# Kernel optimization log

Hardware: AMD Instinct MI355X
Metric: run time of the kernel (lower is better)

The kernel has to match this reference:

```python
import jax, jax.numpy as jnp
import numpy as np

N_NODES = 50_000
N_EDGES = 1_600_000
D = 128          # input_dim == hidden_dim
L = 3            # num_layers
NUM_GRAPHS = 64
LN_EPS = 1e-5


def setup_inputs() -> dict:
    key = jax.random.key(0)
    ks = jax.random.split(key, 12)
    x = jax.random.normal(ks[0], (N_NODES, D), dtype=jnp.float32)
    edge_index = jax.random.randint(ks[1], (2, N_EDGES), 0, N_NODES, dtype=jnp.int64)
    edge_weight = jax.random.normal(ks[2], (N_EDGES,), dtype=jnp.float32)  # signed
    batch = jnp.sort(jax.random.randint(ks[3], (N_NODES,), 0, NUM_GRAPHS, dtype=jnp.int64))
    W_pos = jax.random.normal(ks[4], (L, D, D), dtype=jnp.float32) * 0.05
    b_pos = jnp.zeros((L, D), dtype=jnp.float32)
    W_neg = jax.random.normal(ks[5], (L, D, D), dtype=jnp.float32) * 0.05
    b_neg = jnp.zeros((L, D), dtype=jnp.float32)
    ln_gamma = jnp.ones((D,), dtype=jnp.float32)
    ln_beta = jnp.zeros((D,), dtype=jnp.float32)
    return dict(x=x, edge_index=edge_index, edge_weight=edge_weight, batch=batch,
                W_pos=W_pos, b_pos=b_pos, W_neg=W_neg, b_neg=b_neg,
                ln_gamma=ln_gamma, ln_beta=ln_beta)


def gcn_conv(x, src, dst, w, W, b):
    """PyG GCNConv with edge weights: lin -> sym-normalized scatter-add -> +bias.
    Self-loops (weight 1) are handled analytically instead of appending edges.
    Edges with weight 0 contribute nothing (equivalent to sign-masking the edge set)."""
    n = x.shape[0]
    xw = x @ W                                              # [N, D]
    deg = jax.ops.segment_sum(w, dst, num_segments=n) + 1.0  # +1 for self-loop; >= 1
    dinv = jax.lax.rsqrt(deg)                                # deg^{-1/2}
    norm = dinv[src] * w * dinv[dst]                         # [E]
    agg = jax.ops.segment_sum(norm[:, None] * xw[src], dst, num_segments=n)
    agg = agg + (dinv * dinv)[:, None] * xw                  # self-loop message: xw / deg
    return agg + b


def reference(x, edge_index, edge_weight, batch, W_pos, b_pos, W_neg, b_neg, ln_gamma, ln_beta):
    src, dst = edge_index[0], edge_index[1]
    # sign-split as zero-weight edges: identical math to boolean-masked edge subsets
    w_pos = jnp.maximum(edge_weight, 0.0)
    w_neg = jnp.maximum(-edge_weight, 0.0)
    for l in range(L):
        px = gcn_conv(x, src, dst, w_pos, W_pos[l], b_pos[l])
        nx = gcn_conv(x, src, dst, w_neg, W_neg[l], b_neg[l])
        x = jax.nn.relu(px) - jax.nn.relu(nx)
    # global_mean_pool
    sums = jax.ops.segment_sum(x, batch, num_segments=NUM_GRAPHS)
    counts = jax.ops.segment_sum(jnp.ones((x.shape[0],), x.dtype), batch, num_segments=NUM_GRAPHS)
    pooled = sums / jnp.maximum(counts, 1.0)[:, None]        # [G, D]
    # LayerNorm over feature dim
    mu = pooled.mean(-1, keepdims=True)
    var = ((pooled - mu) ** 2).mean(-1, keepdims=True)
    return (pooled - mu) * jax.lax.rsqrt(var + LN_EPS) * ln_gamma + ln_beta
```

## Files before the change

kernel.cpp:

```cpp
#include <hip/hip_runtime.h>
#include <hip/hip_fp16.h>

#define D 128
#define NG 64
#define WPB 4
#define TILE 2048
#define BSH 6
#define BNODES 64
#define CAP 3072
#define MASK40 ((1ULL << 40) - 1)
#define FPSCALE 1048576.0f
#define INV_FPSCALE (1.0f / 1048576.0f)
typedef unsigned int uint;
typedef unsigned long long u64;
typedef _Float16 f16x8 __attribute__((ext_vector_type(8)));
typedef float f32x4 __attribute__((ext_vector_type(4)));

__global__ void k_prep(const float* __restrict__ x, __half* __restrict__ xo,
                       const float* __restrict__ Wp, const float* __restrict__ Wn,
                       __half* __restrict__ wpt, __half* __restrict__ wnt,
                       float* sums, float* cnt, int* bktcur,
                       int total2, int nbuk) {
    int i = blockIdx.x * blockDim.x + threadIdx.x;
    if (i < total2) {
        float2 f = ((const float2*)x)[i];
        ((__half2*)xo)[i] = __floats2half2_rn(f.x, f.y);
    }
    if (i < 3 * 128 * 128) {
        int l = i >> 14;
        int r = i & 16383;
        int col = r >> 7, k = r & 127;
        size_t src = ((size_t)l << 14) + ((size_t)k << 7) + col;
        wpt[i] = __float2half_rn(Wp[src]);
        wnt[i] = __float2half_rn(Wn[src]);
    }
    if (i < NG * D) sums[i] = 0.0f;
    if (i < NG) cnt[i] = 0.0f;
    if (i < nbuk) bktcur[i] = i * CAP;
}

__global__ __launch_bounds__(256) void k_bucket(const int* __restrict__ ei,
                                                const float* __restrict__ ew,
                                                int* bktcur, uint2* rec,
                                                int E, int nbuk) {
    __shared__ int h[1024];
    __shared__ int cur[1024];
    int t = threadIdx.x;
    for (int b = t; b < 1024; b += 256) h[b] = 0;
    __syncthreads();
    int lo = blockIdx.x * TILE, hi = min(E, lo + TILE);
    for (int e = lo + t; e < hi; e += 256)
        atomicAdd(&h[ei[(size_t)E + e] >> BSH], 1);
    __syncthreads();
    for (int b = t; b < nbuk; b += 256)
        if (h[b]) cur[b] = atomicAdd(&bktcur[b], h[b]);
    __syncthreads();
    for (int e = lo + t; e < hi; e += 256) {
        int dst = ei[(size_t)E + e];
        int src = ei[e];
        float w = ew[e];
        int bkt = dst >> BSH;
        int pos = atomicAdd(&cur[bkt], 1);
        if (pos < (bkt + 1) * CAP)
            rec[pos] = make_uint2((uint)src | ((uint)(dst & (BNODES - 1)) << 16),
                                  __float_as_uint(w));
    }
}

__global__ __launch_bounds__(256) void k_deg(const uint2* __restrict__ rec,
                                             const int* __restrict__ bktcur,
                                             float2* dpn, int* row_ptr,
                                             int* cend, int* cpos, int n) {
    __shared__ u64 accp[BNODES], accn[BNODES];
    int b = blockIdx.x, t = threadIdx.x;
    if (t < BNODES) { accp[t] = 0ULL; accn[t] = 0ULL; }
    __syncthreads();
    int lo = b * CAP, hi = bktcur[b];
    for (int i = lo + t; i < hi; i += 256) {
        uint2 r = rec[i];
        int dl = (r.x >> 16) & (BNODES - 1);
        float w = __uint_as_float(r.y);
        u64 pkt = (1ULL << 40) | (u64)(fabsf(w) * FPSCALE + 0.5f);
        atomicAdd((w < 0.0f) ? &accn[dl] : &accp[dl], pkt);
    }
    __syncthreads();
    if (t < BNODES) {
        u64 p = accp[t], q = accn[t];
        int cp = (int)(p >> 40), cn = (int)(q >> 40);
        int cnt_t = cp + cn;
        int v = cnt_t;
        for (int off = 1; off < BNODES; off <<= 1) {
            int u = __shfl_up(v, off);
            if (t >= off) v += u;
        }
        int node = b * BNODES + t;
        if (node < n) {
            int base = b * CAP + v - cnt_t;
            row_ptr[node] = base;
            cend[node] = base + cnt_t;
            cpos[node] = cp;
            float2 dd;
            dd.x = rsqrtf(1.0f + (float)(p & MASK40) * INV_FPSCALE);
            dd.y = rsqrtf(1.0f + (float)(q & MASK40) * INV_FPSCALE);
            dpn[node] = dd;
        }
    }
}

__global__ __launch_bounds__(256) void k_csr(const uint2* __restrict__ rec,
                                             const int* __restrict__ bktcur,
                                             const int* __restrict__ row_ptr,
                                             const int* __restrict__ cpos,
                                             const float2* __restrict__ dpn,
                                             uint* pack, int n) {
    __shared__ int curp[BNODES], curn[BNODES];
    int b = blockIdx.x, t = threadIdx.x;
    if (t < BNODES) {
        int node = b * BNODES + t;
        if (node < n) {
            int rp = row_ptr[node];
            curp[t] = rp;
            curn[t] = rp + cpos[node];
        } else { curp[t] = 0; curn[t] = 0; }
    }
    __syncthreads();
    int lo = b * CAP, hi = bktcur[b];
    for (int i = lo + t; i < hi; i += 256) {
        uint2 r = rec[i];
        int src = r.x & 0xFFFFu;
        int dl = (r.x >> 16) & (BNODES - 1);
        float w = __uint_as_float(r.y);
        float2 dd = dpn[src];
        float v;
        int slot;
        if (w < 0.0f) { v = dd.y * (-w); slot = atomicAdd(&curn[dl], 1); }
        else          { v = dd.x * w;    slot = atomicAdd(&curp[dl], 1); }
        pack[slot] = (uint)src | ((uint)__half_as_ushort(__float2half_rn(v)) << 16);
    }
}

__global__ __launch_bounds__(64 * WPB) void k_gather(
    const __half* __restrict__ x16, const uint* __restrict__ pack,
    const int* __restrict__ row_ptr, const int* __restrict__ cend,
    const int* __restrict__ cpos, const float2* __restrict__ dpn,
    __half* __restrict__ tp, __half* __restrict__ tn, int n) {
    __shared__ uint eb[WPB][136];
    const int w = threadIdx.x >> 6;
    const int lane = threadIdx.x & 63;
    const int q = lane >> 4;
    const int c = lane & 15;
    const int node = blockIdx.x * WPB + w;
    if (node >= n) return;
    const int beg = row_ptr[node], end = cend[node];
    const int mid = beg + cpos[node];
    const float2 dd = dpn[node];
    const uint4* __restrict__ x4u = (const uint4*)x16;
    uint* ebw = eb[w];

    uint4 xv = x4u[(size_t)node * 16 + c];
    float xf[8];
    {
        float2 f;
        f = __half22float2(*(__half2*)&xv.x); xf[0] = f.x; xf[1] = f.y;
        f = __half22float2(*(__half2*)&xv.y); xf[2] = f.x; xf[3] = f.y;
        f = __half22float2(*(__half2*)&xv.z); xf[4] = f.x; xf[5] = f.y;
        f = __half22float2(*(__half2*)&xv.w); xf[6] = f.x; xf[7] = f.y;
    }

#pragma unroll
    for (int part = 0; part < 2; ++part) {
        const int lo = part ? mid : beg;
        const int hi = part ? end : mid;
        const float ds = part ? dd.y : dd.x;
        float a0[8], a1[8];
        const float s0 = (q == 0) ? ds : 0.0f;
#pragma unroll
        for (int j = 0; j < 8; ++j) { a0[j] = s0 * xf[j]; a1[j] = 0.0f; }
        for (int cb = lo; cb < hi; cb += 128) {
            int m = hi - cb;
            if (m > 128) m = 128;
            const int mp = (m + 7) & ~7;
            for (int i = lane; i < mp; i += 64)
                ebw[i] = (i < m) ? pack[cb + i] : 0u;
            for (int i = 0; i < mp; i += 8) {
                const uint pk0 = ebw[i + q];
                const uint pk1 = ebw[i + 4 + q];
                const uint4 y0 = x4u[(size_t)(pk0 & 0xFFFFu) * 16 + c];
                const uint4 y1 = x4u[(size_t)(pk1 & 0xFFFFu) * 16 + c];
                const float v0 =
                    __half2float(__ushort_as_half((unsigned short)(pk0 >> 16)));
                const float v1 =
                    __half2float(__ushort_as_half((unsigned short)(pk1 >> 16)));
                float2 f;
                f = __half22float2(*(__half2*)&y0.x);
                a0[0] = fmaf(v0, f.x, a0[0]); a0[1] = fmaf(v0, f.y, a0[1]);
                f = __half22float2(*(__half2*)&y0.y);
                a0[2] = fmaf(v0, f.x, a0[2]); a0[3] = fmaf(v0, f.y, a0[3]);
                f = __half22float2(*(__half2*)&y0.z);
                a0[4] = fmaf(v0, f.x, a0[4]); a0[5] = fmaf(v0, f.y, a0[5]);
                f = __half22float2(*(__half2*)&y0.w);
                a0[6] = fmaf(v0, f.x, a0[6]); a0[7] = fmaf(v0, f.y, a0[7]);
                f = __half22float2(*(__half2*)&y1.x);
                a1[0] = fmaf(v1, f.x, a1[0]); a1[1] = fmaf(v1, f.y, a1[1]);
                f = __half22float2(*(__half2*)&y1.y);
                a1[2] = fmaf(v1, f.x, a1[2]); a1[3] = fmaf(v1, f.y, a1[3]);
                f = __half22float2(*(__half2*)&y1.z);
                a1[4] = fmaf(v1, f.x, a1[4]); a1[5] = fmaf(v1, f.y, a1[5]);
                f = __half22float2(*(__half2*)&y1.w);
                a1[6] = fmaf(v1, f.x, a1[6]); a1[7] = fmaf(v1, f.y, a1[7]);
            }
        }
#pragma unroll
        for (int j = 0; j < 8; ++j) {
            a0[j] += a1[j];
            a0[j] += __shfl_down(a0[j], 32);
            a0[j] += __shfl_down(a0[j], 16);
        }
        if (q == 0) {
            __half2 h0 = __floats2half2_rn(ds * a0[0], ds * a0[1]);
            __half2 h1 = __floats2half2_rn(ds * a0[2], ds * a0[3]);
            __half2 h2 = __floats2half2_rn(ds * a0[4], ds * a0[5]);
            __half2 h3 = __floats2half2_rn(ds * a0[6], ds * a0[7]);
            uint4 st;
            st.x = *(uint*)&h0; st.y = *(uint*)&h1;
            st.z = *(uint*)&h2; st.w = *(uint*)&h3;
            ((uint4*)(part ? tn : tp))[(size_t)node * 16 + c] = st;
        }
    }
}

__global__ __launch_bounds__(256) void k_gemm(
    const __half* __restrict__ tp, const __half* __restrict__ tn,
    const __half* __restrict__ wpt, const __half* __restrict__ wnt,
    const float* __restrict__ bp, const float* __restrict__ bn,
    __half* __restrict__ xout, int nrows) {
    const int wave = threadIdx.x >> 6;
    const int lane = threadIdx.x & 63;
    const int cl = lane & 15;
    const int quad = lane >> 4;
    const int row_blk = blockIdx.x * 64 + wave * 16;
    if (row_blk >= nrows) return;
    int arow = row_blk + cl;
    if (arow >= nrows) arow = nrows - 1;
    const f16x8* __restrict__ tpr = (const f16x8*)(tp + (size_t)arow * 128);
    const f16x8* __restrict__ tnr = (const f16x8*)(tn + (size_t)arow * 128);
    f16x8 ap[4], an[4];
#pragma unroll
    for (int kb = 0; kb < 4; ++kb) {
        ap[kb] = tpr[kb * 4 + quad];
        an[kb] = tnr[kb * 4 + quad];
    }
#pragma unroll
    for (int ct = 0; ct < 8; ++ct) {
        const int col = ct * 16 + cl;
        const f16x8* __restrict__ wpr = (const f16x8*)(wpt + (size_t)col * 128);
        const f16x8* __restrict__ wnr = (const f16x8*)(wnt + (size_t)col * 128);
        f32x4 accp = {0.0f, 0.0f, 0.0f, 0.0f};
        f32x4 accn = {0.0f, 0.0f, 0.0f, 0.0f};
#pragma unroll
        for (int kb = 0; kb < 4; ++kb) {
            accp = __builtin_amdgcn_mfma_f32_16x16x32_f16(ap[kb], wpr[kb * 4 + quad],
                                                          accp, 0, 0, 0);
            accn = __builtin_amdgcn_mfma_f32_16x16x32_f16(an[kb], wnr[kb * 4 + quad],
                                                          accn, 0, 0, 0);
        }
        const float bpv = bp[col], bnv = bn[col];
#pragma unroll
        for (int reg = 0; reg < 4; ++reg) {
            int row = row_blk + quad * 4 + reg;
            if (row < nrows) {
                float pv = accp[reg] + bpv;
                float nv = accn[reg] + bnv;
                xout[(size_t)row * 128 + col] =
                    __float2half_rn(fmaxf(pv, 0.0f) - fmaxf(nv, 0.0f));
            }
        }
    }
}

__global__ __launch_bounds__(128) void k_pool(
    const __half* __restrict__ x, const int* __restrict__ batch,
    float* sums, float* cnt, int n) {
    int f = threadIdx.x;
    int n0 = blockIdx.x * 64;
    int n1 = min(n0 + 64, n);
    float acc = 0.0f;
    int g_prev = batch[n0];
    int local = 0;
    for (int i = n0; i < n1; ++i) {
        int g = batch[i];
        if (g != g_prev) {
            atomicAdd(&sums[g_prev * D + f], acc);
            if (f == 0) atomicAdd(&cnt[g_prev], (float)local);
            acc = 0.0f; local = 0; g_prev = g;
        }
        acc += __half2float(x[(size_t)i * D + f]);
        local++;
    }
    atomicAdd(&sums[g_prev * D + f], acc);
    if (f == 0) atomicAdd(&cnt[g_prev], (float)local);
}

__global__ __launch_bounds__(128) void k_ln(
    const float* __restrict__ sums, const float* __restrict__ cnt,
    const float* __restrict__ gamma, const float* __restrict__ beta,
    float* __restrict__ out) {
    __shared__ float red[128];
    int g = blockIdx.x, f = threadIdx.x;
    float c = fmaxf(cnt[g], 1.0f);
    float v = sums[g * D + f] / c;
    red[f] = v;
    __syncthreads();
    for (int off = 64; off > 0; off >>= 1) {
        if (f < off) red[f] += red[f + off];
        __syncthreads();
    }
    float mu = red[0] / (float)D;
    __syncthreads();
    float d = v - mu;
    red[f] = d * d;
    __syncthreads();
    for (int off = 64; off > 0; off >>= 1) {
        if (f < off) red[f] += red[f + off];
        __syncthreads();
    }
    float var = red[0] / (float)D;
    out[g * D + f] = d * rsqrtf(var + 1e-5f) * gamma[f] + beta[f];
}

extern "C" void kernel_launch(void* const* d_in, const int* in_sizes, int n_in,
                              void* d_out, int out_size, void* d_ws,
                              size_t ws_size, hipStream_t stream) {
    const float* x     = (const float*)d_in[0];
    const int*   ei    = (const int*)d_in[1];
    const float* ew    = (const float*)d_in[2];
    const int*   bat   = (const int*)d_in[3];
    const float* Wp    = (const float*)d_in[4];
    const float* bp    = (const float*)d_in[5];
    const float* Wn    = (const float*)d_in[6];
    const float* bn    = (const float*)d_in[7];
    const float* gamma = (const float*)d_in[8];
    const float* beta  = (const float*)d_in[9];
    const int n = in_sizes[0] / D;
    const int E = in_sizes[2];
    const int NBUK = (n + BNODES - 1) >> BSH;
    const int NBLK = (E + TILE - 1) / TILE;

    float* ws = (float*)d_ws;
    size_t off = 0;
    auto alloc = [&](size_t elems) {
        float* p = ws + off;
        off += (elems + 63) & ~(size_t)63;
        return p;
    };
    __half* x16  = (__half*)alloc((size_t)n * D / 2);
    __half* tpb  = (__half*)alloc((size_t)n * D / 2);
    __half* tnb  = (__half*)alloc((size_t)n * D / 2);
    __half* xb   = (__half*)alloc((size_t)n * D / 2);
    __half* wpt  = (__half*)alloc(3 * 128 * 128 / 2);
    __half* wnt  = (__half*)alloc(3 * 128 * 128 / 2);
    float2* dpn  = (float2*)alloc((size_t)2 * n);
    float* sums  = alloc(NG * D);
    float* cnt   = alloc(NG);
    int* bktcur  = (int*)alloc(NBUK);
    int* row_ptr = (int*)alloc(n);
    int* cend    = (int*)alloc(n);
    int* cpos    = (int*)alloc(n);
    uint2* rec   = (uint2*)alloc((size_t)NBUK * CAP * 2);
    uint* pack   = (uint*)alloc((size_t)NBUK * CAP);

    k_prep<<<(n * D / 2 + 255) / 256, 256, 0, stream>>>(
        x, x16, Wp, Wn, wpt, wnt, sums, cnt, bktcur, n * D / 2, NBUK);
    k_bucket<<<NBLK, 256, 0, stream>>>(ei, ew, bktcur, rec, E, NBUK);
    k_deg<<<NBUK, 256, 0, stream>>>(rec, bktcur, dpn, row_ptr, cend, cpos, n);
    k_csr<<<NBUK, 256, 0, stream>>>(rec, bktcur, row_ptr, cpos, dpn, pack, n);

    const __half* xcur = x16;
    for (int l = 0; l < 3; ++l) {
        k_gather<<<(n + WPB - 1) / WPB, 64 * WPB, 0, stream>>>(
            xcur, pack, row_ptr, cend, cpos, dpn, tpb, tnb, n);
        k_gemm<<<(n + 63) / 64, 256, 0, stream>>>(
            tpb, tnb, wpt + (size_t)l * 128 * 128, wnt + (size_t)l * 128 * 128,
            bp + (size_t)l * D, bn + (size_t)l * D, xb, n);
        xcur = xb;
    }
    k_pool<<<(n + 63) / 64, 128, 0, stream>>>(xb, bat, sums, cnt, n);
    k_ln<<<NG, 128, 0, stream>>>(sums, cnt, gamma, beta, (float*)d_out);
}
```

Baseline: 445.9 us.

## Enlarge destination buckets to 128 nodes and stage GEMM weights in LDS

Bucket size grows from 64 to 128 destination nodes, with a larger edge tile and capacity per bucket. This halves the bucket count and the number of degree/CSR blocks, so the prefix scan in k_deg becomes a shared-memory scan with block-wide syncs instead of a single-wavefront shuffle. Separately, the GEMM kernel now copies both fp16 weight matrices into padded LDS once per block and reads MFMA B-operands from there rather than from global memory. This adds about 70KB of LDS per block, which can reduce occupancy, and the larger buckets raise the risk of overflowing CAP on skewed degree distributions.

```diff
diff --git a/kernel.cpp b/kernel.cpp
--- a/kernel.cpp
+++ b/kernel.cpp
@@ -4,10 +4,10 @@
 #define D 128
 #define NG 64
 #define WPB 4
-#define TILE 2048
-#define BSH 6
-#define BNODES 64
-#define CAP 3072
+#define TILE 4096
+#define BSH 7
+#define BNODES 128
+#define CAP 4608
 #define MASK40 ((1ULL << 40) - 1)
 #define FPSCALE 1048576.0f
 #define INV_FPSCALE (1.0f / 1048576.0f)
@@ -43,10 +43,10 @@
                                                 const float* __restrict__ ew,
                                                 int* bktcur, uint2* rec,
                                                 int E, int nbuk) {
-    __shared__ int h[1024];
-    __shared__ int cur[1024];
+    __shared__ int h[512];
+    __shared__ int cur[512];
     int t = threadIdx.x;
-    for (int b = t; b < 1024; b += 256) h[b] = 0;
+    for (int b = t; b < 512; b += 256) h[b] = 0;
     __syncthreads();
     int lo = blockIdx.x * TILE, hi = min(E, lo + TILE);
     for (int e = lo + t; e < hi; e += 256)
@@ -72,6 +72,7 @@
                                              float2* dpn, int* row_ptr,
                                              int* cend, int* cpos, int n) {
     __shared__ u64 accp[BNODES], accn[BNODES];
+    __shared__ int s[BNODES];
     int b = blockIdx.x, t = threadIdx.x;
     if (t < BNODES) { accp[t] = 0ULL; accn[t] = 0ULL; }
     __syncthreads();
@@ -84,18 +85,26 @@
         atomicAdd((w < 0.0f) ? &accn[dl] : &accp[dl], pkt);
     }
     __syncthreads();
+    int cp = 0, cn = 0, cnt_t = 0;
+    u64 p = 0, q = 0;
     if (t < BNODES) {
-        u64 p = accp[t], q = accn[t];
-        int cp = (int)(p >> 40), cn = (int)(q >> 40);
-        int cnt_t = cp + cn;
-        int v = cnt_t;
-        for (int off = 1; off < BNODES; off <<= 1) {
-            int u = __shfl_up(v, off);
-            if (t >= off) v += u;
-        }
+        p = accp[t]; q = accn[t];
+        cp = (int)(p >> 40); cn = (int)(q >> 40);
+        cnt_t = cp + cn;
+        s[t] = cnt_t;
+    }
+    __syncthreads();
+    for (int off = 1; off < BNODES; off <<= 1) {
+        int u = 0;
+        if (t < BNODES && t >= off) u = s[t - off];
+        __syncthreads();
+        if (t < BNODES) s[t] += u;
+        __syncthreads();
+    }
+    if (t < BNODES) {
         int node = b * BNODES + t;
         if (node < n) {
-            int base = b * CAP + v - cnt_t;
+            int base = b * CAP + s[t] - cnt_t;
             row_ptr[node] = base;
             cend[node] = base + cnt_t;
             cpos[node] = cp;
@@ -234,11 +243,26 @@
     const __half* __restrict__ wpt, const __half* __restrict__ wnt,
     const float* __restrict__ bp, const float* __restrict__ bn,
     __half* __restrict__ xout, int nrows) {
-    const int wave = threadIdx.x >> 6;
-    const int lane = threadIdx.x & 63;
+    __shared__ __half wlds[2][128][136];
+    const int tid = threadIdx.x;
+    {
+        const uint4* wp4 = (const uint4*)wpt;
+        const uint4* wn4 = (const uint4*)wnt;
+#pragma unroll
+        for (int j = 0; j < 8; ++j) {
+            int idx = tid + j * 256;
+            int col = idx >> 4;
+            int k8 = idx & 15;
+            *(uint4*)&wlds[0][col][k8 * 8] = wp4[idx];
+            *(uint4*)&wlds[1][col][k8 * 8] = wn4[idx];
+        }
+    }
+    const int wave = tid >> 6;
+    const int lane = tid & 63;
     const int cl = lane & 15;
     const int quad = lane >> 4;
     const int row_blk = blockIdx.x * 64 + wave * 16;
+    __syncthreads();
     if (row_blk >= nrows) return;
     int arow = row_blk + cl;
     if (arow >= nrows) arow = nrows - 1;
@@ -253,16 +277,14 @@
 #pragma unroll
     for (int ct = 0; ct < 8; ++ct) {
         const int col = ct * 16 + cl;
-        const f16x8* __restrict__ wpr = (const f16x8*)(wpt + (size_t)col * 128);
-        const f16x8* __restrict__ wnr = (const f16x8*)(wnt + (size_t)col * 128);
         f32x4 accp = {0.0f, 0.0f, 0.0f, 0.0f};
         f32x4 accn = {0.0f, 0.0f, 0.0f, 0.0f};
 #pragma unroll
         for (int kb = 0; kb < 4; ++kb) {
-            accp = __builtin_amdgcn_mfma_f32_16x16x32_f16(ap[kb], wpr[kb * 4 + quad],
-                                                          accp, 0, 0, 0);
-            accn = __builtin_amdgcn_mfma_f32_16x16x32_f16(an[kb], wnr[kb * 4 + quad],
-                                                          accn, 0, 0, 0);
+            f16x8 wfp = *(const f16x8*)&wlds[0][col][kb * 32 + quad * 8];
+            f16x8 wfn = *(const f16x8*)&wlds[1][col][kb * 32 + quad * 8];
+            accp = __builtin_amdgcn_mfma_f32_16x16x32_f16(ap[kb], wfp, accp, 0, 0, 0);
+            accn = __builtin_amdgcn_mfma_f32_16x16x32_f16(an[kb], wfn, accn, 0, 0, 0);
         }
         const float bpv = bp[col], bnv = bn[col];
 #pragma unroll
```

Result: faster. 395.4 us (-11.3%).
